# Kernel optimization log

Hardware: AMD Instinct MI355X
Metric: run time of the kernel (lower is better)

## Reference

```python
import jax, jax.numpy as jnp
import numpy as np

EPS = 1e-8      # covariance regularizer (module-level `eps` in source repo)
ALPHA = 0.8     # style/content blend (module-level `alpha` in source repo)
SV_THRESH = 1e-5  # singular-value cutoff from the source


def _flatten(x):
    # x: [1, H, W, C] -> [C, H*W]
    xt = jnp.transpose(x[0], (2, 0, 1))  # C, H, W
    C = xt.shape[0]
    return xt.reshape(C, -1)


def _cov(f):
    # f: [C, N] already centered -> [C, C]
    C, N = f.shape
    return f @ f.T / (jnp.float32(N) - 1.0) + EPS * jnp.eye(C, dtype=f.dtype)


def _masked_pow(S, p):
    # Faithful to truncating columns with S <= 1e-5: zero their diag weight.
    mask = S > SV_THRESH
    S_safe = jnp.where(mask, S, 1.0)
    return jnp.where(mask, S_safe ** p, 0.0)


def setup_inputs() -> dict:
    key = jax.random.key(0)
    k1, k2 = jax.random.split(key)
    content = jax.random.normal(k1, (1, 128, 128, 512), dtype=jnp.float32)
    style = jax.random.normal(k2, (1, 128, 128, 512), dtype=jnp.float32)
    return {"content": content, "style": style}


def reference(content, style):
    H, W, C = content.shape[1], content.shape[2], content.shape[3]

    content_flat = _flatten(content)  # [C, Hc*Wc]
    style_flat = _flatten(style)      # [C, Hs*Ws]

    mc = content_flat.mean(axis=1, keepdims=True)
    fc = content_flat - mc
    ms = style_flat.mean(axis=1, keepdims=True)
    fs = style_flat - ms

    fcfc = _cov(fc)
    fsfs = _cov(fs)

    # tf.svd on a symmetric PSD matrix: S descending, U orthonormal.
    Uc, Sc, _ = jnp.linalg.svd(fcfc)
    Us, Ss, _ = jnp.linalg.svd(fsfs)

    # Whitening: Uc diag(Sc^-1/2) Uc^T (truncated cols == zeroed diag entries)
    Dc = _masked_pow(Sc, -0.5)
    whiten = (Uc * Dc[None, :]) @ Uc.T  # [C, C]
    fc_hat = whiten @ fc                # [C, N]

    # Coloring: Us diag(Ss^1/2) Us^T
    Ds = _masked_pow(Ss, 0.5)
    color = (Us * Ds[None, :]) @ Us.T
    fcs_hat = color @ fc_hat + ms

    blended = ALPHA * fcs_hat + (1.0 - ALPHA) * (fc + mc)  # [C, N]
    blended = blended.reshape(C, H, W)
    return jnp.transpose(blended, (1, 2, 0))[None]  # [1, H, W, C]
```

## Files before the change

### kernel.cpp

```cpp
#include <hip/hip_runtime.h>
#include <math.h>

#define NPIX 16384
#define CCH  512
#define MS   262144

typedef unsigned short u16;
typedef unsigned int u32;
typedef __attribute__((ext_vector_type(8))) short bf16x8;
typedef __attribute__((ext_vector_type(4))) float f32x4;

__device__ __forceinline__ u16 f2bf(float f) {
  u32 u = __builtin_bit_cast(u32, f);
  u += 0x7fffu + ((u >> 16) & 1u);
  return (u16)(u >> 16);
}
__device__ __forceinline__ float b2f(u16 h) {
  u32 u = ((u32)h) << 16;
  return __builtin_bit_cast(float, u);
}

typedef const __attribute__((address_space(1))) u32* gp_t;
typedef __attribute__((address_space(3))) u32* lp_t;
__device__ __forceinline__ void gl_lds16(const void* g, void* l) {
  __builtin_amdgcn_global_load_lds((gp_t)g, (lp_t)l, 16, 0, 0);
}

__device__ __forceinline__ void stage4(const u16* tile, size_t stride, int rl,
                                       int k0, u16* lds, int lane) {
  int lr = lane >> 4;
  int cg = (lane & 15) ^ ((rl + lr) & 15);
  gl_lds16(tile + (size_t)(rl + lr) * stride + k0 + cg * 8,
           lds + (size_t)rl * 128);
}
__device__ __forceinline__ bf16x8 fragld(const u16* lds, int row, int cl) {
  return *(const bf16x8*)&lds[(size_t)row * 128 + (size_t)((cl ^ (row & 15)) << 3)];
}

__device__ __forceinline__ void stage8_64(const u16* tile, size_t stride, int rl,
                                          int k0, u16* lds, int lane) {
  int lr = lane >> 3;
  int cg = (lane & 7) ^ ((rl + lr) & 7);
  gl_lds16(tile + (size_t)(rl + lr) * stride + k0 + cg * 8,
           lds + (size_t)rl * 64);
}
__device__ __forceinline__ bf16x8 fragld64(const u16* lds, int row, int cl) {
  return *(const bf16x8*)&lds[(size_t)row * 64 + (size_t)((cl ^ (row & 7)) << 3)];
}

__global__ __launch_bounds__(256) void prep_k(const float* __restrict__ Xc,
                                              const float* __restrict__ Xs,
                                              float* __restrict__ sums,
                                              u16* __restrict__ fct,
                                              u16* __restrict__ fcb) {
  int b = blockIdx.z;
  const float* X = b ? Xs : Xc;
  u16* outT = fct + (size_t)b * ((size_t)CCH * NPIX);
  __shared__ float T[64][65];
  __shared__ float red2[64][4];
  int n0 = blockIdx.x * 64, c0 = blockIdx.y * 64;
  int t = threadIdx.x;
  int cr = t & 15, nr = t >> 4;
  #pragma unroll
  for (int rr = 0; rr < 4; ++rr) {
    int n = nr + rr * 16;
    float4 v = *(const float4*)&X[(size_t)(n0 + n) * CCH + c0 + cr * 4];
    T[n][cr * 4 + 0] = v.x;
    T[n][cr * 4 + 1] = v.y;
    T[n][cr * 4 + 2] = v.z;
    T[n][cr * 4 + 3] = v.w;
    if (b == 0) {
      ushort4 q;
      q.x = f2bf(v.x); q.y = f2bf(v.y); q.z = f2bf(v.z); q.w = f2bf(v.w);
      *(ushort4*)&fcb[(size_t)(n0 + n) * CCH + c0 + cr * 4] = q;
    }
  }
  __syncthreads();
  int cl = t >> 2, np = (t & 3) * 16;
  size_t obase = (size_t)(c0 + cl) * NPIX + n0 + np;
  float s = 0.f;
  #pragma unroll
  for (int i = 0; i < 16; i += 4) {
    float v0 = T[np + i + 0][cl], v1 = T[np + i + 1][cl];
    float v2 = T[np + i + 2][cl], v3 = T[np + i + 3][cl];
    s += v0 + v1 + v2 + v3;
    ushort4 o;
    o.x = f2bf(v0); o.y = f2bf(v1); o.z = f2bf(v2); o.w = f2bf(v3);
    *(ushort4*)&outT[obase + i] = o;
  }
  red2[cl][t & 3] = s;
  __syncthreads();
  if (t < 64) {
    float cs = red2[t][0] + red2[t][1] + red2[t][2] + red2[t][3];
    atomicAdd(&sums[b * CCH + c0 + t], cs);
  }
}

__global__ __launch_bounds__(256, 4) void gram_part(const u16* __restrict__ fct,
                                                    float* __restrict__ Gp) {
  int kc = blockIdx.x;
  int pair = blockIdx.y;
  int b = blockIdx.z;
  int bi = pair >> 2, bj = pair & 3;
  const u16* Xb = fct + (size_t)b * ((size_t)CCH * NPIX);
  __shared__ u16 As[128 * 64];
  __shared__ u16 Bs[128 * 64];
  int tid = threadIdx.x, w = tid >> 6, lane = tid & 63;
  int qm = w & 1, qn = w >> 1;
  const u16* ssrc = (w < 2) ? Xb + (size_t)(bi * 128) * NPIX
                            : Xb + (size_t)(bj * 128) * NPIX;
  u16* sdst = (w < 2) ? As : Bs;
  int rbase = (w & 1) * 64;
  f32x4 acc[4][4];
  #pragma unroll
  for (int t = 0; t < 4; ++t)
    #pragma unroll
    for (int u = 0; u < 4; ++u) acc[t][u] = (f32x4)(0.f);

  for (int st = 0; st < 16; ++st) {
    int k0 = kc * 1024 + st * 64;
    __syncthreads();
    #pragma unroll
    for (int i = 0; i < 8; ++i) stage8_64(ssrc, NPIX, rbase + i * 8, k0, sdst, lane);
    __syncthreads();
    #pragma unroll
    for (int s = 0; s < 2; ++s) {
      int cl = s * 4 + (lane >> 4);
      bf16x8 a[4], bb[4];
      #pragma unroll
      for (int t = 0; t < 4; ++t) a[t] = fragld64(As, qm * 64 + t * 16 + (lane & 15), cl);
      #pragma unroll
      for (int u = 0; u < 4; ++u) bb[u] = fragld64(Bs, qn * 64 + u * 16 + (lane & 15), cl);
      #pragma unroll
      for (int t = 0; t < 4; ++t)
        #pragma unroll
        for (int u = 0; u < 4; ++u)
          acc[t][u] = __builtin_amdgcn_mfma_f32_16x16x32_bf16(a[t], bb[u], acc[t][u], 0, 0, 0);
    }
  }
  size_t tbase = ((size_t)(b * 16 + kc) * 16 + pair) * 16384;
  #pragma unroll
  for (int t = 0; t < 4; ++t) {
    int row0 = qm * 64 + t * 16 + (lane >> 4) * 4;
    #pragma unroll
    for (int u = 0; u < 4; ++u) {
      int col = qn * 64 + u * 16 + (lane & 15);
      #pragma unroll
      for (int r4 = 0; r4 < 4; ++r4)
        Gp[tbase + (size_t)(row0 + r4) * 128 + col] = acc[t][u][r4];
    }
  }
}

__global__ __launch_bounds__(256) void gram_reduce(const float* __restrict__ Gp,
                                                   const float* __restrict__ sums,
                                                   float* __restrict__ cov,
                                                   float* __restrict__ rowsum) {
  int idx = blockIdx.x * 256 + threadIdx.x;
  int b = idx >> 18;
  int ij = idx & (MS - 1);
  int i = ij >> 9, j = ij & 511;
  int pair = ((i >> 7) << 2) | (j >> 7);
  int lij = ((i & 127) << 7) | (j & 127);
  size_t base = ((size_t)(b * 16) * 16 + pair) * 16384 + lij;
  float g = 0.f;
  #pragma unroll
  for (int kc = 0; kc < 16; ++kc)
    g += Gp[base + (size_t)kc * (16 * 16384)];
  const float* s = sums + b * CCH;
  float v = (g - s[i] * s[j] * (1.f / (float)NPIX)) * (1.f / (float)(NPIX - 1));
  if (i == j) v += 1e-8f;
  cov[idx] = v;
  __shared__ float red[256];
  int t = threadIdx.x;
  red[t] = fabsf(v);
  __syncthreads();
  for (int st = 128; st > 0; st >>= 1) {
    if (t < st) red[t] += red[t + st];
    __syncthreads();
  }
  if (t == 0) atomicAdd(&rowsum[b * CCH + i], red[0]);
}

__global__ __launch_bounds__(256) void nsinit_k(const float* __restrict__ cov,
                                                const float* __restrict__ rowsum,
                                                float* __restrict__ snorm,
                                                float* __restrict__ coef,
                                                u16* __restrict__ Anh,
                                                u16* __restrict__ Anl,
                                                u16* __restrict__ Z0) {
  __shared__ float red[256];
  int tid = threadIdx.x, blk = blockIdx.x;
  float m = fmaxf(rowsum[tid], rowsum[tid + 256]);
  red[tid] = m; __syncthreads();
  for (int s = 128; s > 0; s >>= 1) {
    if (tid < s) red[tid] = fmaxf(red[tid], red[tid + s]);
    __syncthreads();
  }
  float snc = red[0]; __syncthreads();
  m = fmaxf(rowsum[512 + tid], rowsum[768 + tid]);
  red[tid] = m; __syncthreads();
  for (int s = 128; s > 0; s >>= 1) {
    if (tid < s) red[tid] = fmaxf(red[tid], red[tid + s]);
    __syncthreads();
  }
  float sns = red[0];
  if (blk == 0 && tid == 0) {
    snorm[0] = snc; snorm[1] = sns;
    coef[0] = 0.8f * sqrtf(sns / snc);
  }
  int idx = blk * 256 + tid;
  int b = idx >> 18;
  int ij = idx & (MS - 1);
  int diag = (ij >> 9) == (ij & 511);
  float av = cov[idx] * (b ? 1.f / sns : 1.f / snc);
  u16 hi = f2bf(av);
  Anh[idx] = hi;
  Anl[idx] = f2bf(av - b2f(hi));
  float t0 = (diag ? 3.f - av : -av) * 0.70710678f;
  Z0[idx] = f2bf(t0);
}

struct MM16 {
  const u16* A[4];
  const u16* B[4];
  void* D[4];
  float scale, diag;
  int outFp32;
};

__global__ __launch_bounds__(256) void mm16_k(MM16 args) {
  int z = blockIdx.z;
  const u16* __restrict__ A = args.A[z];
  const u16* __restrict__ B = args.B[z];
  int bi = blockIdx.y, bj = blockIdx.x;
  __shared__ u16 As[64 * 128];
  __shared__ u16 Bs[64 * 128];
  int tid = threadIdx.x, w = tid >> 6, lane = tid & 63;
  int qm = w & 1, qn = w >> 1;
  const u16* ssrc = ((w < 2) ? A + (size_t)(bi * 64) * CCH : B + (size_t)(bj * 64) * CCH);
  u16* sdst = (w < 2) ? As : Bs;
  int rbase = (w & 1) * 32;
  f32x4 acc[2][2];
  #pragma unroll
  for (int t = 0; t < 2; ++t)
    #pragma unroll
    for (int u = 0; u < 2; ++u) acc[t][u] = (f32x4)(0.f);

  for (int st = 0; st < 4; ++st) {
    int k0 = st * 128;
    __syncthreads();
    #pragma unroll
    for (int i = 0; i < 8; ++i) stage4(ssrc, CCH, rbase + i * 4, k0, sdst, lane);
    __syncthreads();
    #pragma unroll
    for (int s = 0; s < 4; ++s) {
      int cl = s * 4 + (lane >> 4);
      bf16x8 a[2], bb[2];
      #pragma unroll
      for (int t = 0; t < 2; ++t) a[t] = fragld(As, qm * 32 + t * 16 + (lane & 15), cl);
      #pragma unroll
      for (int u = 0; u < 2; ++u) bb[u] = fragld(Bs, qn * 32 + u * 16 + (lane & 15), cl);
      #pragma unroll
      for (int t = 0; t < 2; ++t)
        #pragma unroll
        for (int u = 0; u < 2; ++u)
          acc[t][u] = __builtin_amdgcn_mfma_f32_16x16x32_bf16(a[t], bb[u], acc[t][u], 0, 0, 0);
    }
  }
  float sc = args.scale;
  #pragma unroll
  for (int t = 0; t < 2; ++t) {
    int row0 = bi * 64 + qm * 32 + t * 16 + (lane >> 4) * 4;
    #pragma unroll
    for (int u = 0; u < 2; ++u) {
      int col = bj * 64 + qn * 32 + u * 16 + (lane & 15);
      #pragma unroll
      for (int r4 = 0; r4 < 4; ++r4) {
        float v = sc * acc[t][u][r4];
        if (row0 + r4 == col) v += args.diag;
        size_t o = (size_t)(row0 + r4) * CCH + col;
        if (args.outFp32) ((float*)args.D[z])[o] = v;
        else ((u16*)args.D[z])[o] = f2bf(v);
      }
    }
  }
}

__global__ __launch_bounds__(256) void symsplit_k(const float* __restrict__ src,
                                                  u16* __restrict__ hi,
                                                  u16* __restrict__ lo) {
  int b = blockIdx.y;
  int ij = blockIdx.x * 256 + threadIdx.x;
  int i = ij >> 9, j = ij & 511;
  size_t base = (size_t)b * MS;
  float v = 0.5f * (src[base + ij] + src[base + (size_t)j * CCH + i]);
  u16 h = f2bf(v);
  hi[base + ij] = h;
  lo[base + ij] = f2bf(v - b2f(h));
}

struct MMS {
  const u16 *Ah[4], *Al[4], *Bh[4], *Bl[4];
  const u16 *Eh[4], *El[4];
  u16 *Dh[4], *Dl[4];
  float *D32[4];
  u16 *Db[4];
  float scale, beta;
  const float* coefPtr;
};

__global__ __launch_bounds__(256) void mmsplit_k(MMS args) {
  int z = blockIdx.z;
  int bi = blockIdx.y, bj = blockIdx.x;
  __shared__ u16 Ash[64 * 128], Asl[64 * 128], Bsh[64 * 128], Bsl[64 * 128];
  int tid = threadIdx.x, w = tid >> 6, lane = tid & 63;
  int qm = w & 1, qn = w >> 1;
  const u16* sp = (w == 0) ? args.Ah[z] : (w == 1) ? args.Al[z]
                : (w == 2) ? args.Bh[z] : args.Bl[z];
  const u16* ssrc = sp + (size_t)(((w < 2) ? bi : bj) * 64) * CCH;
  u16* sdst = (w == 0) ? Ash : (w == 1) ? Asl : (w == 2) ? Bsh : Bsl;
  f32x4 acc[2][2];
  #pragma unroll
  for (int t = 0; t < 2; ++t)
    #pragma unroll
    for (int u = 0; u < 2; ++u) acc[t][u] = (f32x4)(0.f);

  for (int st = 0; st < 4; ++st) {
    int k0 = st * 128;
    __syncthreads();
    #pragma unroll
    for (int i = 0; i < 16; ++i) stage4(ssrc, CCH, i * 4, k0, sdst, lane);
    __syncthreads();
    #pragma unroll
    for (int s = 0; s < 4; ++s) {
      int cl = s * 4 + (lane >> 4);
      bf16x8 ah[2], al[2], bh[2], bl[2];
      #pragma unroll
      for (int t = 0; t < 2; ++t) {
        int row = qm * 32 + t * 16 + (lane & 15);
        ah[t] = fragld(Ash, row, cl);
        al[t] = fragld(Asl, row, cl);
      }
      #pragma unroll
      for (int u = 0; u < 2; ++u) {
        int row = qn * 32 + u * 16 + (lane & 15);
        bh[u] = fragld(Bsh, row, cl);
        bl[u] = fragld(Bsl, row, cl);
      }
      #pragma unroll
      for (int t = 0; t < 2; ++t)
        #pragma unroll
        for (int u = 0; u < 2; ++u) {
          acc[t][u] = __builtin_amdgcn_mfma_f32_16x16x32_bf16(ah[t], bh[u], acc[t][u], 0, 0, 0);
          acc[t][u] = __builtin_amdgcn_mfma_f32_16x16x32_bf16(ah[t], bl[u], acc[t][u], 0, 0, 0);
          acc[t][u] = __builtin_amdgcn_mfma_f32_16x16x32_bf16(al[t], bh[u], acc[t][u], 0, 0, 0);
        }
    }
  }
  float sc = args.scale;
  if (args.coefPtr) sc *= *args.coefPtr;
  #pragma unroll
  for (int t = 0; t < 2; ++t) {
    int row0 = bi * 64 + qm * 32 + t * 16 + (lane >> 4) * 4;
    #pragma unroll
    for (int u = 0; u < 2; ++u) {
      int col = bj * 64 + qn * 32 + u * 16 + (lane & 15);
      #pragma unroll
      for (int r4 = 0; r4 < 4; ++r4) {
        size_t o = (size_t)(row0 + r4) * CCH + col;
        float v = sc * acc[t][u][r4];
        if (args.beta != 0.f) v += args.beta * (b2f(args.Eh[z][o]) + b2f(args.El[z][o]));
        if (args.D32[z]) args.D32[z][o] = v;
        if (args.Dh[z]) {
          u16 h = f2bf(v);
          args.Dh[z][o] = h;
          args.Dl[z][o] = f2bf(v - b2f(h));
        }
        if (args.Db[z]) args.Db[z][o] = f2bf(v);
      }
    }
  }
}

__global__ __launch_bounds__(256) void mconst_k(const u16* __restrict__ Mb,
                                                const float* __restrict__ sums,
                                                float* __restrict__ mconst) {
  int c = blockIdx.x * 8 + (threadIdx.x >> 5);
  int l = threadIdx.x & 31;
  float s = 0.f;
  #pragma unroll
  for (int k = 0; k < 16; ++k) {
    int j = l + 32 * k;
    s += b2f(Mb[(size_t)c * CCH + j]) * sums[j];
  }
  s += __shfl_down(s, 16, 32);
  s += __shfl_down(s, 8, 32);
  s += __shfl_down(s, 4, 32);
  s += __shfl_down(s, 2, 32);
  s += __shfl_down(s, 1, 32);
  if (l == 0) mconst[c] = (0.8f * sums[512 + c] - s) * (1.f / (float)NPIX);
}

__global__ __launch_bounds__(256) void apply_mfma(const u16* __restrict__ fcb,
                                                  const u16* __restrict__ Mb,
                                                  const float* __restrict__ mconst,
                                                  const float* __restrict__ X,
                                                  float* __restrict__ out) {
  int bi = blockIdx.y;
  int bj = blockIdx.x;
  __shared__ u16 As[128 * 128];
  __shared__ u16 Bs[128 * 128];
  int tid = threadIdx.x, w = tid >> 6, lane = tid & 63;
  int qm = w & 1, qn = w >> 1;
  const u16* ssrc = (w < 2) ? fcb + (size_t)(bi * 128) * CCH
                            : Mb + (size_t)(bj * 128) * CCH;
  u16* sdst = (w < 2) ? As : Bs;
  int rbase = (w & 1) * 64;
  f32x4 acc[4][4];
  #pragma unroll
  for (int t = 0; t < 4; ++t)
    #pragma unroll
    for (int u = 0; u < 4; ++u) acc[t][u] = (f32x4)(0.f);

  for (int st = 0; st < 4; ++st) {
    int k0 = st * 128;
    __syncthreads();
    #pragma unroll
    for (int i = 0; i < 16; ++i) stage4(ssrc, CCH, rbase + i * 4, k0, sdst, lane);
    __syncthreads();
    #pragma unroll
    for (int s = 0; s < 4; ++s) {
      int cl = s * 4 + (lane >> 4);
      bf16x8 a[4], bb[4];
      #pragma unroll
      for (int t = 0; t < 4; ++t) a[t] = fragld(As, qm * 64 + t * 16 + (lane & 15), cl);
      #pragma unroll
      for (int u = 0; u < 4; ++u) bb[u] = fragld(Bs, qn * 64 + u * 16 + (lane & 15), cl);
      #pragma unroll
      for (int t = 0; t < 4; ++t)
        #pragma unroll
        for (int u = 0; u < 4; ++u)
          acc[t][u] = __builtin_amdgcn_mfma_f32_16x16x32_bf16(a[t], bb[u], acc[t][u], 0, 0, 0);
    }
  }
  #pragma unroll
  for (int t = 0; t < 4; ++t) {
    int row0 = bi * 128 + qm * 64 + t * 16 + (lane >> 4) * 4;
    #pragma unroll
    for (int u = 0; u < 4; ++u) {
      int col = bj * 128 + qn * 64 + u * 16 + (lane & 15);
      float cst = mconst[col];
      #pragma unroll
      for (int r4 = 0; r4 < 4; ++r4) {
        size_t o = (size_t)(row0 + r4) * CCH + col;
        out[o] = acc[t][u][r4] + cst + 0.2f * X[o];
      }
    }
  }
}

extern "C" void kernel_launch(void* const* d_in, const int* in_sizes, int n_in,
                              void* d_out, int out_size, void* d_ws, size_t ws_size,
                              hipStream_t stream) {
  const float* Xc = (const float*)d_in[0];
  const float* Xs = (const float*)d_in[1];
  float* out = (float*)d_out;

  float* f = (float*)d_ws;
  float* sums   = f;
  float* rowsum = f + 1024;
  float* cov    = f + 2048 + 2 * MS;
  float* snorm  = cov + 2 * MS;
  float* coef   = snorm + 8;
  float* mconst = coef + 8;
  float* Zf     = mconst + 512;

  float* Gp = (float*)d_out;

  u16* h   = (u16*)(Zf + 2 * MS);
  u16* fct = h;
  u16* fcb = h + (size_t)2 * CCH * NPIX;
  const size_t B2 = 2 * MS;
  u16* Anh  = fct + 0 * B2;
  u16* Anl  = fct + 1 * B2;
  u16* Y1   = fct + 2 * B2;
  u16* Ya   = fct + 3 * B2;
  u16* Z0   = fct + 4 * B2;
  u16* Z1   = fct + 5 * B2;
  u16* Tb   = fct + 6 * B2;
  u16* Zfsh = fct + 7 * B2;
  u16* Zfsl = fct + 8 * B2;
  u16* Ph   = fct + 9 * B2;
  u16* Pl   = fct + 10 * B2;
  u16* Qh   = fct + 11 * B2;
  u16* Ql   = fct + 12 * B2;
  u16* Zrsh = fct + 13 * B2;
  u16* Zrsl = fct + 14 * B2;
  u16* W2h  = fct + 15 * B2;
  u16* W2l  = W2h + MS;
  u16* Mb   = W2l + MS;

  hipMemsetAsync(d_ws, 0, 2048 * sizeof(float), stream);

  prep_k<<<dim3(256, 8, 2), 256, 0, stream>>>(Xc, Xs, sums, fct, fcb);
  gram_part<<<dim3(16, 16, 2), 256, 0, stream>>>(fct, Gp);
  gram_reduce<<<2048, 256, 0, stream>>>(Gp, sums, cov, rowsum);
  nsinit_k<<<2048, 256, 0, stream>>>(cov, rowsum, snorm, coef, Anh, Anl, Z0);

  {
    MM16 y1{};
    y1.A[0] = Anh;      y1.B[0] = Z0;      y1.D[0] = Y1;
    y1.A[1] = Anh + MS; y1.B[1] = Z0 + MS; y1.D[1] = Y1 + MS;
    y1.scale = 1.f; y1.diag = 0.f; y1.outFp32 = 0;
    mm16_k<<<dim3(8, 8, 2), 256, 0, stream>>>(y1);
  }
  {
    MM16 t{};
    t.A[0] = Z0;      t.B[0] = Y1;      t.D[0] = Tb;
    t.A[1] = Z0 + MS; t.B[1] = Y1 + MS; t.D[1] = Tb + MS;
    t.scale = -1.f; t.diag = 3.f; t.outFp32 = 0;
    mm16_k<<<dim3(8, 8, 2), 256, 0, stream>>>(t);
  }
  {
    MM16 yz{};
    yz.A[0] = Y1;      yz.B[0] = Tb;      yz.D[0] = Ya;
    yz.A[1] = Y1 + MS; yz.B[1] = Tb + MS; yz.D[1] = Ya + MS;
    yz.A[2] = Tb;      yz.B[2] = Z0;      yz.D[2] = Z1;
    yz.A[3] = Tb + MS; yz.B[3] = Z0 + MS; yz.D[3] = Z1 + MS;
    yz.scale = 0.5f; yz.diag = 0.f; yz.outFp32 = 0;
    mm16_k<<<dim3(8, 8, 4), 256, 0, stream>>>(yz);
  }
  {
    MM16 t{};
    t.A[0] = Z1;      t.B[0] = Ya;      t.D[0] = Tb;
    t.A[1] = Z1 + MS; t.B[1] = Ya + MS; t.D[1] = Tb + MS;
    t.scale = -1.f; t.diag = 3.f; t.outFp32 = 0;
    mm16_k<<<dim3(8, 8, 2), 256, 0, stream>>>(t);
  }
  {
    MM16 yz{};
    yz.A[0] = Ya;      yz.B[0] = Tb;      yz.D[0] = Y1;
    yz.A[1] = Ya + MS; yz.B[1] = Tb + MS; yz.D[1] = Y1 + MS;
    yz.A[2] = Tb;      yz.B[2] = Z1;      yz.D[2] = Z0;
    yz.A[3] = Tb + MS; yz.B[3] = Z1 + MS; yz.D[3] = Z0 + MS;
    yz.scale = 0.5f; yz.diag = 0.f; yz.outFp32 = 0;
    mm16_k<<<dim3(8, 8, 4), 256, 0, stream>>>(yz);
  }
  {
    MM16 t{};
    t.A[0] = Z0;      t.B[0] = Y1;      t.D[0] = Tb;
    t.A[1] = Z0 + MS; t.B[1] = Y1 + MS; t.D[1] = Tb + MS;
    t.scale = -1.f; t.diag = 3.f; t.outFp32 = 0;
    mm16_k<<<dim3(8, 8, 2), 256, 0, stream>>>(t);
  }
  {
    MM16 zf{};
    zf.A[0] = Tb;      zf.B[0] = Z0;      zf.D[0] = Zf;
    zf.A[1] = Tb + MS; zf.B[1] = Z0 + MS; zf.D[1] = Zf + MS;
    zf.scale = 0.5f; zf.diag = 0.f; zf.outFp32 = 1;
    mm16_k<<<dim3(8, 8, 2), 256, 0, stream>>>(zf);
  }

  symsplit_k<<<dim3(1024, 2), 256, 0, stream>>>(Zf, Zfsh, Zfsl);

  MMS pq{};
  for (int b = 0; b < 2; ++b) {
    pq.Ah[b] = Zfsh + b * MS; pq.Al[b] = Zfsl + b * MS;
    pq.Bh[b] = Anh + b * MS;  pq.Bl[b] = Anl + b * MS;
    pq.Dh[b] = Ph + b * MS;   pq.Dl[b] = Pl + b * MS;
    pq.Ah[2 + b] = Zfsh + b * MS; pq.Al[2 + b] = Zfsl + b * MS;
    pq.Bh[2 + b] = Zfsh + b * MS; pq.Bl[2 + b] = Zfsl + b * MS;
    pq.Dh[2 + b] = Qh + b * MS;   pq.Dl[2 + b] = Ql + b * MS;
  }
  pq.scale = 1.f;
  mmsplit_k<<<dim3(8, 8, 4), 256, 0, stream>>>(pq);

  MMS zr{};
  for (int b = 0; b < 2; ++b) {
    zr.Ah[b] = Ph + b * MS;   zr.Al[b] = Pl + b * MS;
    zr.Bh[b] = Qh + b * MS;   zr.Bl[b] = Ql + b * MS;
    zr.Eh[b] = Zfsh + b * MS; zr.El[b] = Zfsl + b * MS;
    zr.D32[b] = Zf + b * MS;
  }
  zr.scale = -0.5f; zr.beta = 1.5f;
  mmsplit_k<<<dim3(8, 8, 2), 256, 0, stream>>>(zr);

  symsplit_k<<<dim3(1024, 2), 256, 0, stream>>>(Zf, Zrsh, Zrsl);

  MMS wv{};
  wv.Ah[0] = Anh + MS;  wv.Al[0] = Anl + MS;
  wv.Bh[0] = Zrsh + MS; wv.Bl[0] = Zrsl + MS;
  wv.Dh[0] = W2h; wv.Dl[0] = W2l;
  wv.scale = 1.f;
  mmsplit_k<<<dim3(8, 8, 1), 256, 0, stream>>>(wv);

  MMS mv{};
  mv.Ah[0] = W2h;  mv.Al[0] = W2l;
  mv.Bh[0] = Zrsh; mv.Bl[0] = Zrsl;
  mv.Db[0] = Mb;
  mv.scale = 1.f; mv.coefPtr = coef;
  mmsplit_k<<<dim3(8, 8, 1), 256, 0, stream>>>(mv);

  mconst_k<<<64, 256, 0, stream>>>(Mb, sums, mconst);
  apply_mfma<<<dim3(4, 128), 256, 0, stream>>>(fcb, Mb, mconst, Xc, out);
}
```

Before: 279.9 us.

## Double-buffer LDS staging in gram, mm16, mmsplit and apply GEMM kernels

Converts four MFMA GEMM kernels from single-buffered LDS staging with two barriers per k-step to ping-pong double buffering. The next tile's global-to-LDS copy is issued before computing on the current tile, leaving one barrier per step. mmsplit and apply also drop to 64-wide k tiles so the doubled buffers fit in LDS. gram_part's occupancy hint falls from 4 to 2 blocks per CU because of the larger LDS footprint, which may reduce latency hiding.

```diff
diff --git a/kernel.cpp b/kernel.cpp
--- a/kernel.cpp
+++ b/kernel.cpp
@@ -96,20 +96,19 @@
   }
 }
 
-__global__ __launch_bounds__(256, 4) void gram_part(const u16* __restrict__ fct,
+__global__ __launch_bounds__(256, 2) void gram_part(const u16* __restrict__ fct,
                                                     float* __restrict__ Gp) {
   int kc = blockIdx.x;
   int pair = blockIdx.y;
   int b = blockIdx.z;
   int bi = pair >> 2, bj = pair & 3;
   const u16* Xb = fct + (size_t)b * ((size_t)CCH * NPIX);
-  __shared__ u16 As[128 * 64];
-  __shared__ u16 Bs[128 * 64];
+  __shared__ u16 As[2][128 * 64];
+  __shared__ u16 Bs[2][128 * 64];
   int tid = threadIdx.x, w = tid >> 6, lane = tid & 63;
   int qm = w & 1, qn = w >> 1;
   const u16* ssrc = (w < 2) ? Xb + (size_t)(bi * 128) * NPIX
                             : Xb + (size_t)(bj * 128) * NPIX;
-  u16* sdst = (w < 2) ? As : Bs;
   int rbase = (w & 1) * 64;
   f32x4 acc[4][4];
   #pragma unroll
@@ -117,26 +116,35 @@
     #pragma unroll
     for (int u = 0; u < 4; ++u) acc[t][u] = (f32x4)(0.f);
 
+  #pragma unroll
+  for (int i = 0; i < 8; ++i)
+    stage8_64(ssrc, NPIX, rbase + i * 8, kc * 1024, (w < 2) ? As[0] : Bs[0], lane);
+  __syncthreads();
+
   for (int st = 0; st < 16; ++st) {
-    int k0 = kc * 1024 + st * 64;
-    __syncthreads();
-    #pragma unroll
-    for (int i = 0; i < 8; ++i) stage8_64(ssrc, NPIX, rbase + i * 8, k0, sdst, lane);
-    __syncthreads();
+    int cur = st & 1;
+    if (st < 15) {
+      int k0n = kc * 1024 + (st + 1) * 64;
+      #pragma unroll
+      for (int i = 0; i < 8; ++i)
+        stage8_64(ssrc, NPIX, rbase + i * 8, k0n,
+                  (w < 2) ? As[cur ^ 1] : Bs[cur ^ 1], lane);
+    }
     #pragma unroll
     for (int s = 0; s < 2; ++s) {
       int cl = s * 4 + (lane >> 4);
       bf16x8 a[4], bb[4];
       #pragma unroll
-      for (int t = 0; t < 4; ++t) a[t] = fragld64(As, qm * 64 + t * 16 + (lane & 15), cl);
-      #pragma unroll
-      for (int u = 0; u < 4; ++u) bb[u] = fragld64(Bs, qn * 64 + u * 16 + (lane & 15), cl);
+      for (int t = 0; t < 4; ++t) a[t] = fragld64(As[cur], qm * 64 + t * 16 + (lane & 15), cl);
+      #pragma unroll
+      for (int u = 0; u < 4; ++u) bb[u] = fragld64(Bs[cur], qn * 64 + u * 16 + (lane & 15), cl);
       #pragma unroll
       for (int t = 0; t < 4; ++t)
         #pragma unroll
         for (int u = 0; u < 4; ++u)
           acc[t][u] = __builtin_amdgcn_mfma_f32_16x16x32_bf16(a[t], bb[u], acc[t][u], 0, 0, 0);
     }
+    __syncthreads();
   }
   size_t tbase = ((size_t)(b * 16 + kc) * 16 + pair) * 16384;
   #pragma unroll
@@ -234,12 +242,11 @@
   const u16* __restrict__ A = args.A[z];
   const u16* __restrict__ B = args.B[z];
   int bi = blockIdx.y, bj = blockIdx.x;
-  __shared__ u16 As[64 * 128];
-  __shared__ u16 Bs[64 * 128];
+  __shared__ u16 As[2][64 * 128];
+  __shared__ u16 Bs[2][64 * 128];
   int tid = threadIdx.x, w = tid >> 6, lane = tid & 63;
   int qm = w & 1, qn = w >> 1;
   const u16* ssrc = ((w < 2) ? A + (size_t)(bi * 64) * CCH : B + (size_t)(bj * 64) * CCH);
-  u16* sdst = (w < 2) ? As : Bs;
   int rbase = (w & 1) * 32;
   f32x4 acc[2][2];
   #pragma unroll
@@ -247,26 +254,34 @@
     #pragma unroll
     for (int u = 0; u < 2; ++u) acc[t][u] = (f32x4)(0.f);
 
+  #pragma unroll
+  for (int i = 0; i < 8; ++i)
+    stage4(ssrc, CCH, rbase + i * 4, 0, (w < 2) ? As[0] : Bs[0], lane);
+  __syncthreads();
+
   for (int st = 0; st < 4; ++st) {
-    int k0 = st * 128;
-    __syncthreads();
-    #pragma unroll
-    for (int i = 0; i < 8; ++i) stage4(ssrc, CCH, rbase + i * 4, k0, sdst, lane);
-    __syncthreads();
+    int cur = st & 1;
+    if (st < 3) {
+      #pragma unroll
+      for (int i = 0; i < 8; ++i)
+        stage4(ssrc, CCH, rbase + i * 4, (st + 1) * 128,
+               (w < 2) ? As[cur ^ 1] : Bs[cur ^ 1], lane);
+    }
     #pragma unroll
     for (int s = 0; s < 4; ++s) {
       int cl = s * 4 + (lane >> 4);
       bf16x8 a[2], bb[2];
       #pragma unroll
-      for (int t = 0; t < 2; ++t) a[t] = fragld(As, qm * 32 + t * 16 + (lane & 15), cl);
-      #pragma unroll
-      for (int u = 0; u < 2; ++u) bb[u] = fragld(Bs, qn * 32 + u * 16 + (lane & 15), cl);
+      for (int t = 0; t < 2; ++t) a[t] = fragld(As[cur], qm * 32 + t * 16 + (lane & 15), cl);
+      #pragma unroll
+      for (int u = 0; u < 2; ++u) bb[u] = fragld(Bs[cur], qn * 32 + u * 16 + (lane & 15), cl);
       #pragma unroll
       for (int t = 0; t < 2; ++t)
         #pragma unroll
         for (int u = 0; u < 2; ++u)
           acc[t][u] = __builtin_amdgcn_mfma_f32_16x16x32_bf16(a[t], bb[u], acc[t][u], 0, 0, 0);
     }
+    __syncthreads();
   }
   float sc = args.scale;
   #pragma unroll
@@ -313,40 +328,49 @@
 __global__ __launch_bounds__(256) void mmsplit_k(MMS args) {
   int z = blockIdx.z;
   int bi = blockIdx.y, bj = blockIdx.x;
-  __shared__ u16 Ash[64 * 128], Asl[64 * 128], Bsh[64 * 128], Bsl[64 * 128];
+  __shared__ u16 Ash[2][64 * 64], Asl[2][64 * 64];
+  __shared__ u16 Bsh[2][64 * 64], Bsl[2][64 * 64];
   int tid = threadIdx.x, w = tid >> 6, lane = tid & 63;
   int qm = w & 1, qn = w >> 1;
   const u16* sp = (w == 0) ? args.Ah[z] : (w == 1) ? args.Al[z]
                 : (w == 2) ? args.Bh[z] : args.Bl[z];
   const u16* ssrc = sp + (size_t)(((w < 2) ? bi : bj) * 64) * CCH;
-  u16* sdst = (w == 0) ? Ash : (w == 1) ? Asl : (w == 2) ? Bsh : Bsl;
+  u16* sd0 = (w == 0) ? Ash[0] : (w == 1) ? Asl[0] : (w == 2) ? Bsh[0] : Bsl[0];
+  u16* sd1 = (w == 0) ? Ash[1] : (w == 1) ? Asl[1] : (w == 2) ? Bsh[1] : Bsl[1];
   f32x4 acc[2][2];
   #pragma unroll
   for (int t = 0; t < 2; ++t)
     #pragma unroll
     for (int u = 0; u < 2; ++u) acc[t][u] = (f32x4)(0.f);
 
-  for (int st = 0; st < 4; ++st) {
-    int k0 = st * 128;
-    __syncthreads();
-    #pragma unroll
-    for (int i = 0; i < 16; ++i) stage4(ssrc, CCH, i * 4, k0, sdst, lane);
-    __syncthreads();
-    #pragma unroll
-    for (int s = 0; s < 4; ++s) {
+  #pragma unroll
+  for (int i = 0; i < 8; ++i)
+    stage8_64(ssrc, CCH, i * 8, 0, sd0, lane);
+  __syncthreads();
+
+  for (int st = 0; st < 8; ++st) {
+    int cur = st & 1;
+    if (st < 7) {
+      u16* sdn = cur ? sd0 : sd1;
+      #pragma unroll
+      for (int i = 0; i < 8; ++i)
+        stage8_64(ssrc, CCH, i * 8, (st + 1) * 64, sdn, lane);
+    }
+    #pragma unroll
+    for (int s = 0; s < 2; ++s) {
       int cl = s * 4 + (lane >> 4);
       bf16x8 ah[2], al[2], bh[2], bl[2];
       #pragma unroll
       for (int t = 0; t < 2; ++t) {
         int row = qm * 32 + t * 16 + (lane & 15);
-        ah[t] = fragld(Ash, row, cl);
-        al[t] = fragld(Asl, row, cl);
+        ah[t] = fragld64(Ash[cur], row, cl);
+        al[t] = fragld64(Asl[cur], row, cl);
       }
       #pragma unroll
       for (int u = 0; u < 2; ++u) {
         int row = qn * 32 + u * 16 + (lane & 15);
-        bh[u] = fragld(Bsh, row, cl);
-        bl[u] = fragld(Bsl, row, cl);
+        bh[u] = fragld64(Bsh[cur], row, cl);
+        bl[u] = fragld64(Bsl[cur], row, cl);
       }
       #pragma unroll
       for (int t = 0; t < 2; ++t)
@@ -357,6 +381,7 @@
           acc[t][u] = __builtin_amdgcn_mfma_f32_16x16x32_bf16(al[t], bh[u], acc[t][u], 0, 0, 0);
         }
     }
+    __syncthreads();
   }
   float sc = args.scale;
   if (args.coefPtr) sc *= *args.coefPtr;
@@ -409,13 +434,12 @@
                                                   float* __restrict__ out) {
   int bi = blockIdx.y;
   int bj = blockIdx.x;
-  __shared__ u16 As[128 * 128];
-  __shared__ u16 Bs[128 * 128];
+  __shared__ u16 As[2][128 * 64];
+  __shared__ u16 Bs[2][128 * 64];
   int tid = threadIdx.x, w = tid >> 6, lane = tid & 63;
   int qm = w & 1, qn = w >> 1;
   const u16* ssrc = (w < 2) ? fcb + (size_t)(bi * 128) * CCH
                             : Mb + (size_t)(bj * 128) * CCH;
-  u16* sdst = (w < 2) ? As : Bs;
   int rbase = (w & 1) * 64;
   f32x4 acc[4][4];
   #pragma unroll
@@ -423,26 +447,34 @@
     #pragma unroll
     for (int u = 0; u < 4; ++u) acc[t][u] = (f32x4)(0.f);
 
-  for (int st = 0; st < 4; ++st) {
-    int k0 = st * 128;
-    __syncthreads();
-    #pragma unroll
-    for (int i = 0; i < 16; ++i) stage4(ssrc, CCH, rbase + i * 4, k0, sdst, lane);
-    __syncthreads();
-    #pragma unroll
-    for (int s = 0; s < 4; ++s) {
+  #pragma unroll
+  for (int i = 0; i < 8; ++i)
+    stage8_64(ssrc, CCH, rbase + i * 8, 0, (w < 2) ? As[0] : Bs[0], lane);
+  __syncthreads();
+
+  for (int st = 0; st < 8; ++st) {
+    int cur = st & 1;
+    if (st < 7) {
+      #pragma unroll
+      for (int i = 0; i < 8; ++i)
+        stage8_64(ssrc, CCH, rbase + i * 8, (st + 1) * 64,
+                  (w < 2) ? As[cur ^ 1] : Bs[cur ^ 1], lane);
+    }
+    #pragma unroll
+    for (int s = 0; s < 2; ++s) {
       int cl = s * 4 + (lane >> 4);
       bf16x8 a[4], bb[4];
       #pragma unroll
-      for (int t = 0; t < 4; ++t) a[t] = fragld(As, qm * 64 + t * 16 + (lane & 15), cl);
-      #pragma unroll
-      for (int u = 0; u < 4; ++u) bb[u] = fragld(Bs, qn * 64 + u * 16 + (lane & 15), cl);
+      for (int t = 0; t < 4; ++t) a[t] = fragld64(As[cur], qm * 64 + t * 16 + (lane & 15), cl);
+      #pragma unroll
+      for (int u = 0; u < 4; ++u) bb[u] = fragld64(Bs[cur], qn * 64 + u * 16 + (lane & 15), cl);
       #pragma unroll
       for (int t = 0; t < 4; ++t)
         #pragma unroll
         for (int u = 0; u < 4; ++u)
           acc[t][u] = __builtin_amdgcn_mfma_f32_16x16x32_bf16(a[t], bb[u], acc[t][u], 0, 0, 0);
     }
+    __syncthreads();
   }
   #pragma unroll
   for (int t = 0; t < 4; ++t) {
```

Result: no change. 275.5 us (-1.6%).
